# Kernel tuning notes

Hardware: AMD Instinct MI355X
Metric: run time of the kernel (lower is better)

## Reference

```python
import jax, jax.numpy as jnp
import numpy as np

H = 512  # hidden_dimension
B = 32
S = 2048


def setup_inputs() -> dict:
    key = jax.random.key(0)
    k1, k2, k3, k4, k5, k6 = jax.random.split(key, 6)
    decoder_hide = jax.random.normal(k1, (B, H), dtype=jnp.float32)
    encoder_out = jax.random.normal(k2, (B, S, 2 * H), dtype=jnp.float32)
    mask = jax.random.randint(k3, (B, S), 0, 2, dtype=jnp.int32)
    bound = 1.0 / np.sqrt(3 * H)
    W_attn = jax.random.uniform(k4, (3 * H, H), minval=-bound, maxval=bound, dtype=jnp.float32)
    b_attn = jax.random.uniform(k5, (H,), minval=-bound, maxval=bound, dtype=jnp.float32)
    bound_v = 1.0 / np.sqrt(H)
    v_w = jax.random.uniform(k6, (H,), minval=-bound_v, maxval=bound_v, dtype=jnp.float32)
    return {"decoder_hide": decoder_hide, "encoder_out": encoder_out, "mask": mask,
            "W_attn": W_attn, "b_attn": b_attn, "v_w": v_w}


def reference(decoder_hide, encoder_out, mask, W_attn, b_attn, v_w):
    # Split the concat-linear: cat((h, enc)) @ W == h @ W[:H] + enc @ W[H:]
    W_h = W_attn[:H]        # [H, H]
    W_e = W_attn[H:]        # [2H, H]
    dec_proj = decoder_hide @ W_h + b_attn                 # [B, H]
    enc_proj = jnp.einsum('bse,eh->bsh', encoder_out, W_e)  # [B, S, H]
    energy = jnp.tanh(enc_proj + dec_proj[:, None, :])      # [B, S, H]
    attention = jnp.einsum('bsh,h->bs', energy, v_w)        # [B, S]
    attention = jnp.where(mask == 0, jnp.float32(-100000.0), attention)
    return jax.nn.softmax(attention, axis=1)
```

## Files before the change

kernel.cpp:

```cpp
#include <hip/hip_runtime.h>
#include <hip/hip_bf16.h>
#include <math.h>

#define Hdim 512
#define Bdim 32
#define Sdim 2048
#define Kdim 1024
#define Mtot (Bdim * Sdim)

#define BM 64
#define BN 512
#define BK 64

typedef __attribute__((ext_vector_type(8))) short short8;
typedef __attribute__((ext_vector_type(4))) float floatx4;

__device__ __forceinline__ short f2bf(float f) {
    union { float f; unsigned u; } v; v.f = f;
    unsigned r = v.u + 0x7fffu + ((v.u >> 16) & 1u);
    return (short)(r >> 16);
}

__device__ __forceinline__ short8 cvt8(float4 a, float4 b) {
    union { short8 s; __hip_bfloat162 h[4]; } u;
    u.h[0] = __float22bfloat162_rn(make_float2(a.x, a.y));
    u.h[1] = __float22bfloat162_rn(make_float2(a.z, a.w));
    u.h[2] = __float22bfloat162_rn(make_float2(b.x, b.y));
    u.h[3] = __float22bfloat162_rn(make_float2(b.z, b.w));
    return u.s;
}

__device__ __forceinline__ float fast_tanh(float x) {
    float ax = fabsf(x);
    float e  = __expf(-2.0f * ax);
    float r  = (1.0f - e) * __builtin_amdgcn_rcpf(1.0f + e);
    return copysignf(r, x);
}

__global__ __launch_bounds__(256) void prep_kernel(
    const float* __restrict__ W_attn, const float* __restrict__ dec,
    const float* __restrict__ b_attn, short* __restrict__ Wb,
    float* __restrict__ dec_proj)
{
    const int t = threadIdx.x;
    if (blockIdx.x < 512) {
        const float* We = W_attn + Hdim * Hdim;
        __shared__ short tile[32][33];
        const int k0 = (blockIdx.x >> 4) * 32;
        const int n0 = (blockIdx.x & 15) * 32;
        const int r = t >> 5, c = t & 31;
        #pragma unroll
        for (int rr = 0; rr < 4; ++rr)
            tile[r + rr * 8][c] = f2bf(We[(size_t)(k0 + r + rr * 8) * Hdim + n0 + c]);
        __syncthreads();
        #pragma unroll
        for (int rr = 0; rr < 4; ++rr)
            Wb[(size_t)(n0 + r + rr * 8) * Kdim + k0 + c] = tile[c][r + rr * 8];
    } else {
        __shared__ float partl[2][128];
        const int bid = blockIdx.x - 512;
        const int b  = bid >> 2;
        const int cb = bid & 3;
        const int c  = cb * 128 + (t & 127);
        const int kh = t >> 7;
        float acc = 0.0f;
        const int kbeg = kh * 256, kend = kbeg + 256;
        #pragma unroll 8
        for (int k = kbeg; k < kend; ++k)
            acc = fmaf(dec[b * Hdim + k], W_attn[(size_t)k * Hdim + c], acc);
        partl[kh][t & 127] = acc;
        __syncthreads();
        if (t < 128)
            dec_proj[b * Hdim + cb * 128 + t] = partl[0][t] + partl[1][t] + b_attn[cb * 128 + t];
    }
}

__global__ __launch_bounds__(256, 2) void scores_kernel(
    const float* __restrict__ enc,
    const short* __restrict__ Wb,
    const float* __restrict__ dec_proj,
    const float* __restrict__ v_w,
    float* __restrict__ scores)
{
    __shared__ __align__(16) short Asm[BM * BK];
    __shared__ __align__(16) short Bsm[BN * BK];
    __shared__ float redl[BM][4];

    const int t    = threadIdx.x;
    const int row0 = blockIdx.x * BM;
    const int b    = row0 / Sdim;

    const int w    = t >> 6;
    const int lane = t & 63;
    const int ln   = lane & 15;
    const int quad = lane >> 4;

    const int sm = t >> 2;
    const int sq = t & 3;
    const float* Ag = enc + (size_t)(row0 + sm) * Kdim + sq * 16;
    short* Aw = Asm + sm * BK;
    const int aw0 = ((2 * sq)     ^ (sm & 7)) * 8;
    const int aw1 = ((2 * sq + 1) ^ (sm & 7)) * 8;

    const int l3 = lane >> 3, l7 = lane & 7;
    const short* Bg0 = Wb + (size_t)(w * 128 + l3) * Kdim + ((l7 ^ l3) * 8);

    int arow[4], brow[8];
    #pragma unroll
    for (int i = 0; i < 4; ++i) arow[i] = (i * 16 + ln) * BK;
    #pragma unroll
    for (int j = 0; j < 8; ++j) brow[j] = (w * 128 + j * 16 + ln) * BK;
    const int pf0 = (quad       ^ (ln & 7)) * 8;
    const int pf1 = ((4 + quad) ^ (ln & 7)) * 8;

    floatx4 acc[4][8];
    #pragma unroll
    for (int i = 0; i < 4; ++i)
        #pragma unroll
        for (int j = 0; j < 8; ++j)
            acc[i][j] = (floatx4)(0.0f);

    for (int kt = 0; kt < Kdim; kt += BK) {
        __syncthreads();
        #pragma unroll
        for (int r = 0; r < 16; ++r) {
            __builtin_amdgcn_global_load_lds(
                (const __attribute__((address_space(1))) unsigned int*)(const void*)
                    (Bg0 + (size_t)r * 8 * Kdim + kt),
                (__attribute__((address_space(3))) unsigned int*)(void*)
                    (Bsm + (w * 128 + r * 8) * BK),
                16, 0, 0);
        }
        {
            const float4* g = (const float4*)(Ag + kt);
            float4 f0 = g[0], f1 = g[1], f2 = g[2], f3 = g[3];
            *(short8*)&Aw[aw0] = cvt8(f0, f1);
            *(short8*)&Aw[aw1] = cvt8(f2, f3);
        }
        __syncthreads();

        #pragma unroll
        for (int f = 0; f < 2; ++f) {
            const int pf = f ? pf1 : pf0;
            short8 af[4], bfr[8];
            #pragma unroll
            for (int i = 0; i < 4; ++i) af[i]  = *(const short8*)&Asm[arow[i] + pf];
            #pragma unroll
            for (int j = 0; j < 8; ++j) bfr[j] = *(const short8*)&Bsm[brow[j] + pf];
            #pragma unroll
            for (int i = 0; i < 4; ++i)
                #pragma unroll
                for (int j = 0; j < 8; ++j)
                    acc[i][j] = __builtin_amdgcn_mfma_f32_16x16x32_bf16(
                                    af[i], bfr[j], acc[i][j], 0, 0, 0);
        }
    }

    float dpv[8], vwv[8];
    #pragma unroll
    for (int j = 0; j < 8; ++j) {
        int col = w * 128 + j * 16 + ln;
        dpv[j] = dec_proj[b * Hdim + col];
        vwv[j] = v_w[col];
    }
    #pragma unroll
    for (int i = 0; i < 4; ++i) {
        #pragma unroll
        for (int reg = 0; reg < 4; ++reg) {
            float s = 0.0f;
            #pragma unroll
            for (int j = 0; j < 8; ++j) {
                float x = acc[i][j][reg] + dpv[j];
                s = fmaf(vwv[j], fast_tanh(x), s);
            }
            s += __shfl_xor(s, 1, 64);
            s += __shfl_xor(s, 2, 64);
            s += __shfl_xor(s, 4, 64);
            s += __shfl_xor(s, 8, 64);
            if (ln == 0)
                redl[i * 16 + quad * 4 + reg][w] = s;
        }
    }
    __syncthreads();
    if (t < BM)
        scores[row0 + t] = redl[t][0] + redl[t][1] + redl[t][2] + redl[t][3];
}

__global__ __launch_bounds__(256) void softmax_kernel(
    const float* __restrict__ scores, const int* __restrict__ mask,
    float* __restrict__ out)
{
    __shared__ float sred[8];
    const int b = blockIdx.x;
    const int t = threadIdx.x;
    const int lane = t & 63;
    const int wid  = t >> 6;

    float x[8];
    float m = -1e30f;
    #pragma unroll
    for (int j = 0; j < 8; ++j) {
        int idx = b * Sdim + j * 256 + t;
        float v = scores[idx];
        if (mask[idx] == 0) v = -100000.0f;
        x[j] = v;
        m = fmaxf(m, v);
    }
    #pragma unroll
    for (int off = 32; off >= 1; off >>= 1)
        m = fmaxf(m, __shfl_xor(m, off, 64));
    if (lane == 0) sred[wid] = m;
    __syncthreads();
    m = fmaxf(fmaxf(sred[0], sred[1]), fmaxf(sred[2], sred[3]));

    float s = 0.0f;
    #pragma unroll
    for (int j = 0; j < 8; ++j) {
        float e = __expf(x[j] - m);
        x[j] = e;
        s += e;
    }
    #pragma unroll
    for (int off = 32; off >= 1; off >>= 1)
        s += __shfl_xor(s, off, 64);
    if (lane == 0) sred[4 + wid] = s;
    __syncthreads();
    s = sred[4] + sred[5] + sred[6] + sred[7];

    const float inv = 1.0f / s;
    #pragma unroll
    for (int j = 0; j < 8; ++j)
        out[b * Sdim + j * 256 + t] = x[j] * inv;
}

extern "C" void kernel_launch(void* const* d_in, const int* in_sizes, int n_in,
                              void* d_out, int out_size, void* d_ws, size_t ws_size,
                              hipStream_t stream) {
    const float* dec  = (const float*)d_in[0];
    const float* enc  = (const float*)d_in[1];
    const int*   mask = (const int*)  d_in[2];
    const float* W    = (const float*)d_in[3];
    const float* ba   = (const float*)d_in[4];
    const float* vw   = (const float*)d_in[5];
    float* out = (float*)d_out;

    float* dec_proj = (float*)d_ws;
    short* Wb       = (short*)(dec_proj + Bdim * Hdim);
    float* scores   = (float*)(Wb + Hdim * Kdim);

    prep_kernel<<<640, 256, 0, stream>>>(W, dec, ba, Wb, dec_proj);
    scores_kernel<<<Mtot / BM, 256, 0, stream>>>(enc, Wb, dec_proj, vw, scores);
    softmax_kernel<<<Bdim, 256, 0, stream>>>(scores, mask, out);
}
```

Baseline: 429.9 us.

## Load B fragments directly from global memory and double-buffer A in LDS with register prefetch

Removes the LDS staging of the bf16 weight tile. Each wave now reads its MFMA B fragments straight from global memory (L2/cache), which shrinks LDS use and may let more blocks fit per CU. The A tile is double-buffered in LDS and the next tile is prefetched into registers, so only one barrier per K step is needed. In exchange, every block issues redundant global reads of the weights, and the MFMAs now wait on global-load latency instead of LDS latency.

New measurement: 468.8 us. 9.1% more time.

```diff
diff --git a/kernel.cpp b/kernel.cpp
--- a/kernel.cpp
+++ b/kernel.cpp
@@ -82,8 +82,7 @@
     const float* __restrict__ v_w,
     float* __restrict__ scores)
 {
-    __shared__ __align__(16) short Asm[BM * BK];
-    __shared__ __align__(16) short Bsm[BN * BK];
+    __shared__ __align__(16) short Asm[2 * BM * BK];
     __shared__ float redl[BM][4];
 
     const int t    = threadIdx.x;
@@ -98,21 +97,18 @@
     const int sm = t >> 2;
     const int sq = t & 3;
     const float* Ag = enc + (size_t)(row0 + sm) * Kdim + sq * 16;
-    short* Aw = Asm + sm * BK;
+    const int awr = sm * BK;
     const int aw0 = ((2 * sq)     ^ (sm & 7)) * 8;
     const int aw1 = ((2 * sq + 1) ^ (sm & 7)) * 8;
 
-    const int l3 = lane >> 3, l7 = lane & 7;
-    const short* Bg0 = Wb + (size_t)(w * 128 + l3) * Kdim + ((l7 ^ l3) * 8);
-
-    int arow[4], brow[8];
+    int arow[4];
     #pragma unroll
     for (int i = 0; i < 4; ++i) arow[i] = (i * 16 + ln) * BK;
-    #pragma unroll
-    for (int j = 0; j < 8; ++j) brow[j] = (w * 128 + j * 16 + ln) * BK;
     const int pf0 = (quad       ^ (ln & 7)) * 8;
     const int pf1 = ((4 + quad) ^ (ln & 7)) * 8;
 
+    const short* Bl = Wb + (size_t)(w * 128 + ln) * Kdim + quad * 8;
+
     floatx4 acc[4][8];
     #pragma unroll
     for (int i = 0; i < 4; ++i)
@@ -120,33 +116,32 @@
         for (int j = 0; j < 8; ++j)
             acc[i][j] = (floatx4)(0.0f);
 
+    float4 ra0, ra1, ra2, ra3;
+    {
+        const float4* g = (const float4*)Ag;
+        ra0 = g[0]; ra1 = g[1]; ra2 = g[2]; ra3 = g[3];
+    }
+
     for (int kt = 0; kt < Kdim; kt += BK) {
+        short* Ab = Asm + ((kt >> 6) & 1) * (BM * BK);
+        *(short8*)&Ab[awr + aw0] = cvt8(ra0, ra1);
+        *(short8*)&Ab[awr + aw1] = cvt8(ra2, ra3);
         __syncthreads();
-        #pragma unroll
-        for (int r = 0; r < 16; ++r) {
-            __builtin_amdgcn_global_load_lds(
-                (const __attribute__((address_space(1))) unsigned int*)(const void*)
-                    (Bg0 + (size_t)r * 8 * Kdim + kt),
-                (__attribute__((address_space(3))) unsigned int*)(void*)
-                    (Bsm + (w * 128 + r * 8) * BK),
-                16, 0, 0);
+
+        if (kt + BK < Kdim) {
+            const float4* g = (const float4*)(Ag + kt + BK);
+            ra0 = g[0]; ra1 = g[1]; ra2 = g[2]; ra3 = g[3];
         }
-        {
-            const float4* g = (const float4*)(Ag + kt);
-            float4 f0 = g[0], f1 = g[1], f2 = g[2], f3 = g[3];
-            *(short8*)&Aw[aw0] = cvt8(f0, f1);
-            *(short8*)&Aw[aw1] = cvt8(f2, f3);
-        }
-        __syncthreads();
 
         #pragma unroll
         for (int f = 0; f < 2; ++f) {
             const int pf = f ? pf1 : pf0;
             short8 af[4], bfr[8];
             #pragma unroll
-            for (int i = 0; i < 4; ++i) af[i]  = *(const short8*)&Asm[arow[i] + pf];
-            #pragma unroll
-            for (int j = 0; j < 8; ++j) bfr[j] = *(const short8*)&Bsm[brow[j] + pf];
+            for (int j = 0; j < 8; ++j)
+                bfr[j] = *(const short8*)(Bl + (size_t)j * 16 * Kdim + kt + f * 32);
+            #pragma unroll
+            for (int i = 0; i < 4; ++i) af[i] = *(const short8*)&Ab[arow[i] + pf];
             #pragma unroll
             for (int i = 0; i < 4; ++i)
                 #pragma unroll
```
